# Kernel tuning notes

Measured on AMD Instinct MI355X. Metric: run time of the kernel, lower is better.

Reference implementation:

```python
import jax, jax.numpy as jnp
import numpy as np


def _apply1(state, w, m00, m01, m10, m11):
    # state: (N,16) complex64; apply 2x2 gate on wire w (wire 0 = most significant bit)
    st = state.reshape(-1, 2 ** w, 2, 2 ** (3 - w))
    a, b = st[:, :, 0, :], st[:, :, 1, :]
    def bc(v):
        return jnp.reshape(jnp.asarray(v, state.dtype), (-1, 1, 1))
    na = bc(m00) * a + bc(m01) * b
    nb = bc(m10) * a + bc(m11) * b
    return jnp.stack([na, nb], axis=2).reshape(-1, 16)


def _ry(state, theta, w):
    c, s = jnp.cos(theta / 2), jnp.sin(theta / 2)
    return _apply1(state, w, c, -s, s, c)


def _rx(state, theta, w):
    c, s = jnp.cos(theta / 2), jnp.sin(theta / 2)
    return _apply1(state, w, c, -1j * s, -1j * s, c)


def _rz(state, theta, w):
    e = jnp.exp(-0.5j * theta.astype(jnp.complex64))
    return _apply1(state, w, e, 0.0, 0.0, jnp.conj(e))


def _cnot(state, ctrl, tgt):
    s = state.reshape((-1, 2, 2, 2, 2))
    c_ax, t_ax = ctrl + 1, tgt + 1
    s0 = jnp.take(s, 0, axis=c_ax)
    s1 = jnp.take(s, 1, axis=c_ax)
    t2 = t_ax - (1 if t_ax > c_ax else 0)
    s1 = jnp.flip(s1, axis=t2)
    return jnp.stack([s0, s1], axis=c_ax).reshape(-1, 16)


def _measure_z(state):
    # expval of PauliZ on each wire: (N,4)
    p = (state.real ** 2 + state.imag ** 2).reshape(-1, 2, 2, 2, 2)
    z = jnp.array([1.0, -1.0], p.dtype)
    exps = []
    for w in range(4):
        axes = tuple(a for a in (1, 2, 3, 4) if a != w + 1)
        exps.append(p.sum(axes) @ z)
    return jnp.stack(exps, axis=1)


def setup_inputs() -> dict:
    key = jax.random.key(0)
    k = jax.random.split(key, 6)
    B = 2048
    x = jax.random.uniform(k[0], (B, 1, 28, 28), dtype=jnp.float32)
    emb_W = jax.random.normal(k[1], (4, 4), dtype=jnp.float32) * 0.5
    emb_b = jnp.zeros((4,), jnp.float32)
    q_params = jax.random.uniform(k[2], (5,), dtype=jnp.float32, minval=0.0, maxval=2.0 * np.pi)
    lin_W = jax.random.normal(k[3], (10, 784), dtype=jnp.float32) * (1.0 / np.sqrt(784.0))
    lin_b = jnp.zeros((10,), jnp.float32)
    return {"x": x, "emb_W": emb_W, "emb_b": emb_b, "q_params": q_params, "lin_W": lin_W, "lin_b": lin_b}


def reference(x, emb_W, emb_b, q_params, lin_W, lin_b):
    B = x.shape[0]
    img = x.reshape(B, 28, 28)
    # 2x2 non-overlapping patches, row-major over (r, c), ordered [tl, tr, bl, br]
    patches = img.reshape(B, 14, 2, 14, 2).transpose(0, 1, 3, 2, 4).reshape(B, 196, 4)
    ang = (patches @ emb_W.T + emb_b).reshape(-1, 4)  # (B*196, 4)
    N = ang.shape[0]
    state = jnp.zeros((N, 16), jnp.complex64).at[:, 0].set(1.0)
    # data encoding: RY(angle_i) on wire i
    for w in range(4):
        state = _ry(state, ang[:, w], w)
    # fixed 8-op random layer (learnable scalar rotation params + CNOT entanglers)
    state = _rx(state, q_params[0], 0)
    state = _ry(state, q_params[1], 1)
    state = _rz(state, q_params[2], 2)
    state = _cnot(state, 0, 1)
    state = _rx(state, q_params[3], 3)
    state = _cnot(state, 2, 3)
    state = _ry(state, q_params[4], 2)
    state = _cnot(state, 1, 2)
    feats = _measure_z(state).reshape(B, 196 * 4)  # patch-major concat, 4 expvals each
    logits = feats @ lin_W.T + lin_b
    return jax.nn.log_softmax(logits, axis=-1)
```

## Files before the change

kernel.cpp:

```cpp
#include <hip/hip_runtime.h>
#include <hip/hip_bf16.h>


template<int STRIDE>
__device__ __forceinline__ void ry_gate(float re[16], float im[16], float c, float s) {
    #pragma unroll
    for (int base = 0; base < 16; base += 2 * STRIDE) {
        #pragma unroll
        for (int off = 0; off < STRIDE; ++off) {
            const int i0 = base + off, i1 = i0 + STRIDE;
            const float r0 = re[i0], m0 = im[i0], r1 = re[i1], m1 = im[i1];
            re[i0] = c * r0 - s * r1;  im[i0] = c * m0 - s * m1;
            re[i1] = s * r0 + c * r1;  im[i1] = s * m0 + c * m1;
        }
    }
}

template<int STRIDE>
__device__ __forceinline__ void rx_gate(float re[16], float im[16], float c, float s) {
    #pragma unroll
    for (int base = 0; base < 16; base += 2 * STRIDE) {
        #pragma unroll
        for (int off = 0; off < STRIDE; ++off) {
            const int i0 = base + off, i1 = i0 + STRIDE;
            const float r0 = re[i0], m0 = im[i0], r1 = re[i1], m1 = im[i1];
            re[i0] = c * r0 + s * m1;  im[i0] = c * m0 - s * r1;
            re[i1] = s * m0 + c * r1;  im[i1] = -s * r0 + c * m1;
        }
    }
}

template<int STRIDE>
__device__ __forceinline__ void rz_gate(float re[16], float im[16], float c, float s) {
    #pragma unroll
    for (int base = 0; base < 16; base += 2 * STRIDE) {
        #pragma unroll
        for (int off = 0; off < STRIDE; ++off) {
            const int i0 = base + off, i1 = i0 + STRIDE;
            const float r0 = re[i0], m0 = im[i0], r1 = re[i1], m1 = im[i1];
            re[i0] = c * r0 + s * m0;  im[i0] = c * m0 - s * r0;
            re[i1] = c * r1 - s * m1;  im[i1] = s * r1 + c * m1;
        }
    }
}

template<int CMASK, int TMASK>
__device__ __forceinline__ void cnot_gate(float re[16], float im[16]) {
    #pragma unroll
    for (int i = 0; i < 16; ++i) {
        if ((i & CMASK) && !(i & TMASK)) {
            const int j = i | TMASK;
            float t;
            t = re[i]; re[i] = re[j]; re[j] = t;
            t = im[i]; im[i] = im[j]; im[j] = t;
        }
    }
}

__global__ __launch_bounds__(256) void quanv_fused(
    const float* __restrict__ x,
    const float* __restrict__ embW,
    const float* __restrict__ embB,
    const float* __restrict__ qp,
    const float* __restrict__ linW,
    const float* __restrict__ linB,
    float* __restrict__ out)
{
    const int b   = blockIdx.x;
    const int tid = threadIdx.x;

    __shared__ float simg[784];
    __shared__ float sred[4][10];

    const float* img = x + (size_t)b * 784;
    #pragma unroll
    for (int i = 0; i < 4; ++i) {
        const int idx = tid + 256 * i;
        if (idx < 784) simg[idx] = img[idx];
    }
    __syncthreads();

    float part[10];
    #pragma unroll
    for (int c = 0; c < 10; ++c) part[c] = 0.0f;

    if (tid < 196) {
        const int pi = tid / 14, pj = tid % 14;
        const float p0 = simg[(2 * pi) * 28 + 2 * pj];
        const float p1 = simg[(2 * pi) * 28 + 2 * pj + 1];
        const float p2 = simg[(2 * pi + 1) * 28 + 2 * pj];
        const float p3 = simg[(2 * pi + 1) * 28 + 2 * pj + 1];

        float cA[4], sA[4];
        #pragma unroll
        for (int w = 0; w < 4; ++w) {
            const float a = embB[w] + embW[4 * w + 0] * p0 + embW[4 * w + 1] * p1
                                    + embW[4 * w + 2] * p2 + embW[4 * w + 3] * p3;
            __sincosf(0.5f * a, &sA[w], &cA[w]);
        }

        float qc[5], qs[5];
        #pragma unroll
        for (int i = 0; i < 5; ++i) __sincosf(0.5f * qp[i], &qs[i], &qc[i]);

        float re[16], im[16];
        #pragma unroll
        for (int idx = 0; idx < 16; ++idx) {
            float v = 1.0f;
            #pragma unroll
            for (int w = 0; w < 4; ++w)
                v *= ((idx >> (3 - w)) & 1) ? sA[w] : cA[w];
            re[idx] = v;
            im[idx] = 0.0f;
        }

        rx_gate<8>(re, im, qc[0], qs[0]);
        ry_gate<4>(re, im, qc[1], qs[1]);
        rz_gate<2>(re, im, qc[2], qs[2]);
        cnot_gate<8, 4>(re, im);
        rx_gate<1>(re, im, qc[3], qs[3]);
        cnot_gate<2, 1>(re, im);
        ry_gate<2>(re, im, qc[4], qs[4]);
        cnot_gate<4, 2>(re, im);

        float p[16];
        #pragma unroll
        for (int i = 0; i < 16; ++i) p[i] = re[i] * re[i] + im[i] * im[i];
        float f[4];
        #pragma unroll
        for (int w = 0; w < 4; ++w) {
            const int mask = 8 >> w;
            float acc = 0.0f;
            #pragma unroll
            for (int i = 0; i < 16; ++i) acc += (i & mask) ? -p[i] : p[i];
            f[w] = acc;
        }

        #pragma unroll
        for (int c = 0; c < 10; ++c) {
            const float4 wv = *reinterpret_cast<const float4*>(linW + c * 784 + tid * 4);
            part[c] = f[0] * wv.x + f[1] * wv.y + f[2] * wv.z + f[3] * wv.w;
        }
    }

    #pragma unroll
    for (int c = 0; c < 10; ++c) {
        part[c] += __shfl_down(part[c], 32);
        part[c] += __shfl_down(part[c], 16);
        part[c] += __shfl_down(part[c], 8);
        part[c] += __shfl_down(part[c], 4);
        part[c] += __shfl_down(part[c], 2);
        part[c] += __shfl_down(part[c], 1);
    }
    const int lane = tid & 63;
    const int wv   = tid >> 6;
    if (lane == 0) {
        #pragma unroll
        for (int c = 0; c < 10; ++c) sred[wv][c] = part[c];
    }
    __syncthreads();

    if (tid == 0) {
        float logit[10];
        float m = -1e30f;
        #pragma unroll
        for (int c = 0; c < 10; ++c) {
            logit[c] = sred[0][c] + sred[1][c] + sred[2][c] + sred[3][c] + linB[c];
            m = fmaxf(m, logit[c]);
        }
        float ssum = 0.0f;
        #pragma unroll
        for (int c = 0; c < 10; ++c) ssum += expf(logit[c] - m);
        const float lse = m + logf(ssum);
        #pragma unroll
        for (int c = 0; c < 10; ++c) out[(size_t)b * 10 + c] = logit[c] - lse;
    }
}

extern "C" void kernel_launch(void* const* d_in, const int* in_sizes, int n_in,
                              void* d_out, int out_size, void* d_ws, size_t ws_size,
                              hipStream_t stream) {
    const float* x    = (const float*)d_in[0];
    const float* embW = (const float*)d_in[1];
    const float* embB = (const float*)d_in[2];
    const float* qp   = (const float*)d_in[3];
    const float* linW = (const float*)d_in[4];
    const float* linB = (const float*)d_in[5];
    float* out = (float*)d_out;

    const int B = in_sizes[0] / 784;
    quanv_fused<<<B, 256, 0, stream>>>(x, embW, embB, qp, linW, linB, out);
}
```

Measured before the change: 75.43 us.

## Split fused kernel into dense per-patch feature kernel and logits kernel

Splits the single per-image kernel into two launches. The first assigns one thread to each patch across the whole batch, so no lanes sit idle (previously 60 of 256 threads did nothing in the simulation phase). It also computes the Z expectations with a butterfly reduction of shared partial sums. Features go to a workspace buffer, and a second per-image kernel reads them back for the linear layer and log-softmax. The cost is an extra launch plus a global write and read of the features, and the image is read directly from global memory without a shared-memory stage.

New measurement: 81.48 us. +8.0%, slower.

```diff
diff --git a/kernel.cpp b/kernel.cpp
--- a/kernel.cpp
+++ b/kernel.cpp
@@ -57,11 +57,94 @@
     }
 }
 
-__global__ __launch_bounds__(256) void quanv_fused(
+__global__ __launch_bounds__(256) void quanv_feats(
     const float* __restrict__ x,
     const float* __restrict__ embW,
     const float* __restrict__ embB,
     const float* __restrict__ qp,
+    float* __restrict__ feats,
+    int N)
+{
+    const int gid = blockIdx.x * 256 + threadIdx.x;
+    if (gid >= N) return;
+
+    const unsigned b = (unsigned)gid / 196u;
+    const unsigned t = (unsigned)gid % 196u;
+    const unsigned pi = t / 14u, pj = t % 14u;
+
+    const float* img = x + (size_t)b * 784;
+    const float p0 = img[(2 * pi) * 28 + 2 * pj];
+    const float p1 = img[(2 * pi) * 28 + 2 * pj + 1];
+    const float p2 = img[(2 * pi + 1) * 28 + 2 * pj];
+    const float p3 = img[(2 * pi + 1) * 28 + 2 * pj + 1];
+
+    float cA[4], sA[4];
+    #pragma unroll
+    for (int w = 0; w < 4; ++w) {
+        const float a = embB[w] + embW[4 * w + 0] * p0 + embW[4 * w + 1] * p1
+                                + embW[4 * w + 2] * p2 + embW[4 * w + 3] * p3;
+        __sincosf(0.5f * a, &sA[w], &cA[w]);
+    }
+
+    float qc[5], qs[5];
+    #pragma unroll
+    for (int i = 0; i < 5; ++i) __sincosf(0.5f * qp[i], &qs[i], &qc[i]);
+
+    float re[16], im[16];
+    #pragma unroll
+    for (int idx = 0; idx < 16; ++idx) {
+        float v = 1.0f;
+        #pragma unroll
+        for (int w = 0; w < 4; ++w)
+            v *= ((idx >> (3 - w)) & 1) ? sA[w] : cA[w];
+        re[idx] = v;
+        im[idx] = 0.0f;
+    }
+
+    rx_gate<8>(re, im, qc[0], qs[0]);
+    ry_gate<4>(re, im, qc[1], qs[1]);
+    rz_gate<2>(re, im, qc[2], qs[2]);
+    cnot_gate<8, 4>(re, im);
+    rx_gate<1>(re, im, qc[3], qs[3]);
+    cnot_gate<2, 1>(re, im);
+    ry_gate<2>(re, im, qc[4], qs[4]);
+    cnot_gate<4, 2>(re, im);
+
+    float p[16];
+    #pragma unroll
+    for (int i = 0; i < 16; ++i) p[i] = re[i] * re[i] + im[i] * im[i];
+
+    float a8[8], d8;
+    float f0 = 0.0f;
+    #pragma unroll
+    for (int j = 0; j < 8; ++j) {
+        a8[j] = p[j] + p[j + 8];
+        f0 += p[j] - p[j + 8];
+    }
+    float a4[4];
+    float f1 = 0.0f;
+    #pragma unroll
+    for (int j = 0; j < 4; ++j) {
+        a4[j] = a8[j] + a8[j + 4];
+        f1 += a8[j] - a8[j + 4];
+    }
+    float a2[2];
+    float f2 = 0.0f;
+    #pragma unroll
+    for (int j = 0; j < 2; ++j) {
+        a2[j] = a4[j] + a4[j + 2];
+        f2 += a4[j] - a4[j + 2];
+    }
+    const float f3 = a2[0] - a2[1];
+    (void)d8;
+
+    float4 fv;
+    fv.x = f0; fv.y = f1; fv.z = f2; fv.w = f3;
+    *reinterpret_cast<float4*>(feats + (size_t)gid * 4) = fv;
+}
+
+__global__ __launch_bounds__(256) void logits_kernel(
+    const float* __restrict__ feats,
     const float* __restrict__ linW,
     const float* __restrict__ linB,
     float* __restrict__ out)
@@ -69,77 +152,18 @@
     const int b   = blockIdx.x;
     const int tid = threadIdx.x;
 
-    __shared__ float simg[784];
     __shared__ float sred[4][10];
 
-    const float* img = x + (size_t)b * 784;
-    #pragma unroll
-    for (int i = 0; i < 4; ++i) {
-        const int idx = tid + 256 * i;
-        if (idx < 784) simg[idx] = img[idx];
-    }
-    __syncthreads();
-
     float part[10];
     #pragma unroll
     for (int c = 0; c < 10; ++c) part[c] = 0.0f;
 
     if (tid < 196) {
-        const int pi = tid / 14, pj = tid % 14;
-        const float p0 = simg[(2 * pi) * 28 + 2 * pj];
-        const float p1 = simg[(2 * pi) * 28 + 2 * pj + 1];
-        const float p2 = simg[(2 * pi + 1) * 28 + 2 * pj];
-        const float p3 = simg[(2 * pi + 1) * 28 + 2 * pj + 1];
-
-        float cA[4], sA[4];
-        #pragma unroll
-        for (int w = 0; w < 4; ++w) {
-            const float a = embB[w] + embW[4 * w + 0] * p0 + embW[4 * w + 1] * p1
-                                    + embW[4 * w + 2] * p2 + embW[4 * w + 3] * p3;
-            __sincosf(0.5f * a, &sA[w], &cA[w]);
-        }
-
-        float qc[5], qs[5];
-        #pragma unroll
-        for (int i = 0; i < 5; ++i) __sincosf(0.5f * qp[i], &qs[i], &qc[i]);
-
-        float re[16], im[16];
-        #pragma unroll
-        for (int idx = 0; idx < 16; ++idx) {
-            float v = 1.0f;
-            #pragma unroll
-            for (int w = 0; w < 4; ++w)
-                v *= ((idx >> (3 - w)) & 1) ? sA[w] : cA[w];
-            re[idx] = v;
-            im[idx] = 0.0f;
-        }
-
-        rx_gate<8>(re, im, qc[0], qs[0]);
-        ry_gate<4>(re, im, qc[1], qs[1]);
-        rz_gate<2>(re, im, qc[2], qs[2]);
-        cnot_gate<8, 4>(re, im);
-        rx_gate<1>(re, im, qc[3], qs[3]);
-        cnot_gate<2, 1>(re, im);
-        ry_gate<2>(re, im, qc[4], qs[4]);
-        cnot_gate<4, 2>(re, im);
-
-        float p[16];
-        #pragma unroll
-        for (int i = 0; i < 16; ++i) p[i] = re[i] * re[i] + im[i] * im[i];
-        float f[4];
-        #pragma unroll
-        for (int w = 0; w < 4; ++w) {
-            const int mask = 8 >> w;
-            float acc = 0.0f;
-            #pragma unroll
-            for (int i = 0; i < 16; ++i) acc += (i & mask) ? -p[i] : p[i];
-            f[w] = acc;
-        }
-
+        const float4 f = *reinterpret_cast<const float4*>(feats + (size_t)b * 784 + tid * 4);
         #pragma unroll
         for (int c = 0; c < 10; ++c) {
             const float4 wv = *reinterpret_cast<const float4*>(linW + c * 784 + tid * 4);
-            part[c] = f[0] * wv.x + f[1] * wv.y + f[2] * wv.z + f[3] * wv.w;
+            part[c] = f.x * wv.x + f.y * wv.y + f.z * wv.z + f.w * wv.w;
         }
     }
 
@@ -186,8 +210,12 @@
     const float* qp   = (const float*)d_in[3];
     const float* linW = (const float*)d_in[4];
     const float* linB = (const float*)d_in[5];
-    float* out = (float*)d_out;
+    float* out   = (float*)d_out;
+    float* feats = (float*)d_ws;
 
     const int B = in_sizes[0] / 784;
-    quanv_fused<<<B, 256, 0, stream>>>(x, embW, embB, qp, linW, linB, out);
-}
+    const int N = B * 196;
+
+    quanv_feats<<<(N + 255) / 256, 256, 0, stream>>>(x, embW, embB, qp, feats, N);
+    logits_kernel<<<B, 256, 0, stream>>>(feats, linW, linB, out);
+}
```
